# Kernel optimization log

Hardware: AMD Instinct MI355X
Metric: run time of the kernel (lower is better)

## Reference

```python
import jax, jax.numpy as jnp
import numpy as np

B, C_IN, H, W = 8, 1024, 18, 80
FEAT = 1024
A = 32      # anchors per location
NCLS = 3    # classes
NREG = 13
K = 3       # kernel size
K2 = K * K
EPS = 1e-5  # BatchNorm eps


def conv2d(x, w, b):
    y = jax.lax.conv_general_dilated(x, w, (1, 1), ((1, 1), (1, 1)),
                                     dimension_numbers=('NCHW', 'OIHW', 'NCHW'))
    return y + b[None, :, None, None]


def bn_eval(x, g, b):
    # eval-mode BatchNorm2d with running_mean=0, running_var=1
    return x * (g / jnp.sqrt(1.0 + EPS))[None, :, None, None] + b[None, :, None, None]


def anchor_flatten(x, d):
    # [B, A*d, H, W] -> permute(0,2,3,1) -> [B, H*W*A, d]
    Bx, Cx, Hx, Wx = x.shape
    return jnp.transpose(x, (0, 2, 3, 1)).reshape(Bx, Hx * Wx * (Cx // d), d)


def bilinear_gather(x, py, px):
    # x: [B,C,H,W]; py/px: [B,K2,H,W] float coords -> [B,C,K2,H,W], zero outside
    Bx, Cx, Hx, Wx = x.shape
    y0 = jnp.floor(py); x0 = jnp.floor(px)
    wy1 = py - y0; wx1 = px - x0
    wy0 = 1.0 - wy1; wx0 = 1.0 - wx1
    xf = x.reshape(Bx, Cx, Hx * Wx)

    def g(yy, xx):
        valid = ((yy >= 0) & (yy < Hx) & (xx >= 0) & (xx < Wx)).astype(x.dtype)
        yc = jnp.clip(yy, 0, Hx - 1).astype(jnp.int32)
        xc = jnp.clip(xx, 0, Wx - 1).astype(jnp.int32)
        idx = (yc * Wx + xc).reshape(Bx, -1)
        vals = jax.vmap(lambda xi, ii: xi[:, ii])(xf, idx).reshape(Bx, Cx, K2, Hx, Wx)
        return vals * valid[:, None]

    return (g(y0, x0) * (wy0 * wx0)[:, None] + g(y0, x0 + 1) * (wy0 * wx1)[:, None]
            + g(y0 + 1, x0) * (wy1 * wx0)[:, None] + g(y0 + 1, x0 + 1) * (wy1 * wx1)[:, None])


def mdcn(x, off_w, off_b, w, b):
    # ModulatedDeformConvPack (DCNv2): 3x3 conv -> (dy, dx, mask), then modulated deform conv
    out = conv2d(x, off_w, off_b)                        # [B, 3*K2, H, W]
    dy, dx, m = out[:, :K2], out[:, K2:2 * K2], jax.nn.sigmoid(out[:, 2 * K2:])
    ky, kx = jnp.meshgrid(jnp.arange(K, dtype=x.dtype), jnp.arange(K, dtype=x.dtype), indexing='ij')
    base_y = jnp.arange(x.shape[2], dtype=x.dtype)[None, None, :, None] - 1.0 + ky.reshape(1, K2, 1, 1)
    base_x = jnp.arange(x.shape[3], dtype=x.dtype)[None, None, None, :] - 1.0 + kx.reshape(1, K2, 1, 1)
    sampled = bilinear_gather(x, base_y + dy, base_x + dx) * m[:, None]   # [B,C,K2,H,W]
    O = w.shape[0]
    return jnp.einsum('bckhw,ock->bohw', sampled, w.reshape(O, w.shape[1], K2)) + b[None, :, None, None]


def setup_inputs() -> dict:
    key = jax.random.key(0)
    ks = jax.random.split(key, 10)
    s1 = 1.0 / np.sqrt(C_IN * K2)
    s2 = 1.0 / np.sqrt(FEAT * K2)
    rn = lambda k, sh, sc: jax.random.normal(k, sh, jnp.float32) * sc
    return {
        'features': jax.random.normal(ks[0], (B, C_IN, H, W), jnp.float32),
        'cls_w1': rn(ks[1], (FEAT, C_IN, K, K), s1), 'cls_b1': jnp.zeros((FEAT,), jnp.float32),
        'cls_w2': rn(ks[2], (FEAT, FEAT, K, K), s2), 'cls_b2': jnp.zeros((FEAT,), jnp.float32),
        'cls_w3': rn(ks[3], (A * NCLS, FEAT, K, K), s2), 'cls_b3': jnp.zeros((A * NCLS,), jnp.float32),
        'off_w': rn(ks[4], (3 * K2, C_IN, K, K), s1), 'off_b': jnp.zeros((3 * K2,), jnp.float32),
        'dcn_w': rn(ks[5], (FEAT, C_IN, K, K), s1), 'dcn_b': jnp.zeros((FEAT,), jnp.float32),
        'bn1_g': jnp.ones((FEAT,), jnp.float32), 'bn1_b': jnp.zeros((FEAT,), jnp.float32),
        'reg_w2': rn(ks[6], (FEAT, FEAT, K, K), s2), 'reg_b2': jnp.zeros((FEAT,), jnp.float32),
        'bn2_g': jnp.ones((FEAT,), jnp.float32), 'bn2_b': jnp.zeros((FEAT,), jnp.float32),
        'reg_w3': rn(ks[7], (A * NREG, FEAT, K, K), s2), 'reg_b3': jnp.zeros((A * NREG,), jnp.float32),
    }


def reference(features, cls_w1, cls_b1, cls_w2, cls_b2, cls_w3, cls_b3,
              off_w, off_b, dcn_w, dcn_b, bn1_g, bn1_b,
              reg_w2, reg_b2, bn2_g, bn2_b, reg_w3, reg_b3):
    # cls branch (Dropout2d is identity in eval)
    h = jax.nn.relu(conv2d(features, cls_w1, cls_b1))
    h = jax.nn.relu(conv2d(h, cls_w2, cls_b2))
    cls_preds = anchor_flatten(conv2d(h, cls_w3, cls_b3), NCLS)   # [B, H*W*A, NCLS]
    # reg branch: modulated deformable conv -> BN -> ReLU -> conv -> BN -> ReLU -> conv
    r = jax.nn.relu(bn_eval(mdcn(features, off_w, off_b, dcn_w, dcn_b), bn1_g, bn1_b))
    r = jax.nn.relu(bn_eval(conv2d(r, reg_w2, reg_b2), bn2_g, bn2_b))
    reg_preds = anchor_flatten(conv2d(r, reg_w3, reg_b3), NREG)   # [B, H*W*A, NREG]
    return (cls_preds, reg_preds)
```

## Files before the change

kernel.cpp:

```cpp
#include <hip/hip_runtime.h>
#include <math.h>

typedef short short8 __attribute__((ext_vector_type(8)));
typedef float f32x4 __attribute__((ext_vector_type(4)));
typedef unsigned short u16;
typedef unsigned int u32;

#define GAS(p) ((__attribute__((address_space(1))) void*)(p))
#define LAS(p) ((__attribute__((address_space(3))) void*)(p))

namespace {

constexpr int HW   = 1440;
constexpr int PBAT = 20 * 82 * 1024;

__device__ __forceinline__ u16 f2bf(float f) {
  u32 u = __float_as_uint(f);
  return (u16)((u + 0x7FFFu + ((u >> 16) & 1u)) >> 16);
}
__device__ __forceinline__ float bf2f(u16 h) {
  return __uint_as_float(((u32)h) << 16);
}

__device__ __forceinline__ int xcd_virt(int id, int N) {
  int q = N >> 3, r = N & 7;
  int xcd = id & 7, pos = id >> 3;
  return (xcd < r ? xcd * (q + 1) : r * (q + 1) + (xcd - r) * q) + pos;
}

__global__ __launch_bounds__(256)
void transpose_feat(const float* __restrict__ src, u16* __restrict__ dst) {
  __shared__ float tile[128][17];
  const int bh = blockIdx.y;
  const int b = bh / 18, h = bh % 18;
  const int wt = blockIdx.x % 5, ct = blockIdx.x / 5;
  const int w0 = wt * 16, c0 = ct * 128;
  const int tid = threadIdx.x;
#pragma unroll
  for (int it = 0; it < 8; ++it) {
    int idx = it * 256 + tid;
    int c = idx >> 4, w = idx & 15;
    tile[c][w] = src[((size_t)(b * 1024 + c0 + c) * 18 + h) * 80 + w0 + w];
  }
  __syncthreads();
  const int px = tid >> 4, cq = tid & 15;
  union { uint4 u; u16 s[8]; } pk;
#pragma unroll
  for (int j = 0; j < 8; ++j) pk.s[j] = f2bf(tile[cq * 8 + j][px]);
  *(uint4*)(dst + ((size_t)(b * 20 + h + 1) * 82 + (w0 + px + 1)) * 1024 + c0 + cq * 8) = pk.u;
}

struct RepackArgs {
  const float* src[7];
  u16* dst[7];
  int O[7];
  int start[7];
  int nseg;
};

__global__ __launch_bounds__(256)
void repack_all(RepackArgs ra) {
  int blk = blockIdx.x;
  int seg = 0;
#pragma unroll
  for (int i = 1; i < 7; ++i)
    if (i < ra.nseg && blk >= ra.start[i]) seg = i;
  const float* src = ra.src[seg];
  u16* dst = ra.dst[seg];
  const int O = ra.O[seg];
  int idx = (blk - ra.start[seg]) * 256 + threadIdx.x;
  if (idx >= O * 128) return;
  int o = idx >> 7, c8 = idx & 127;
  const float* s = src + (size_t)o * 9216 + (size_t)c8 * 72;
  float v[72];
#pragma unroll
  for (int i = 0; i < 18; ++i) {
    float4 f = *(const float4*)(s + i * 4);
    v[i * 4 + 0] = f.x; v[i * 4 + 1] = f.y; v[i * 4 + 2] = f.z; v[i * 4 + 3] = f.w;
  }
#pragma unroll
  for (int t = 0; t < 9; ++t) {
    union { uint4 u; u16 h[8]; } pk;
#pragma unroll
    for (int j = 0; j < 8; ++j) pk.h[j] = f2bf(v[j * 9 + t]);
    *(uint4*)(dst + ((size_t)t * O + o) * 1024 + c8 * 8) = pk.u;
  }
}

__device__ __forceinline__
void sample_body(int k, int lp, int pix0, int Npc,
                 const u16* __restrict__ featP, const float* __restrict__ offp,
                 u16* __restrict__ spl, int tid) {
  const int p = pix0 + lp;
  const int c8 = tid & 15;
  int b = p / HW, hw = p - b * HW;
  int h = hw / 80, w = hw - h * 80;
  float dy = offp[p * 27 + k];
  float dx = offp[p * 27 + 9 + k];
  float ml = offp[p * 27 + 18 + k];
  float m = 1.f / (1.f + expf(-ml));
  float py = (float)(h - 1 + k / 3) + dy;
  float px = (float)(w - 1 + (k % 3)) + dx;
  float y0f = floorf(py), x0f = floorf(px);
  float wy1 = py - y0f, wx1 = px - x0f;
  float wy0 = 1.f - wy1, wx0 = 1.f - wx1;
  int y0 = (int)y0f, x0 = (int)x0f;
  int ya = min(max(y0, -1), 18),  yb = min(max(y0 + 1, -1), 18);
  int xa = min(max(x0, -1), 80),  xb = min(max(x0 + 1, -1), 80);
  const u16* base = featP + (size_t)b * PBAT;
  const u16* r00 = base + ((size_t)(ya + 1) * 82 + (xa + 1)) * 1024;
  const u16* r01 = base + ((size_t)(ya + 1) * 82 + (xb + 1)) * 1024;
  const u16* r10 = base + ((size_t)(yb + 1) * 82 + (xa + 1)) * 1024;
  const u16* r11 = base + ((size_t)(yb + 1) * 82 + (xb + 1)) * 1024;
  float w00 = wy0 * wx0 * m, w01 = wy0 * wx1 * m;
  float w10 = wy1 * wx0 * m, w11 = wy1 * wx1 * m;
  u16* dst = spl + ((size_t)k * Npc + lp) * 1024;
  for (int c = c8 * 8; c < 1024; c += 128) {
    union { uint4 u; u16 h[8]; } a, bq, cq2, d, o;
    a.u   = *(const uint4*)(r00 + c);
    bq.u  = *(const uint4*)(r01 + c);
    cq2.u = *(const uint4*)(r10 + c);
    d.u   = *(const uint4*)(r11 + c);
#pragma unroll
    for (int j = 0; j < 8; ++j) {
      float v = w00 * bf2f(a.h[j]) + w01 * bf2f(bq.h[j]) +
                w10 * bf2f(cq2.h[j]) + w11 * bf2f(d.h[j]);
      o.h[j] = f2bf(v);
    }
    *(uint4*)(dst + c) = o.u;
  }
}

__global__ __launch_bounds__(256)
void sample_standalone(const u16* __restrict__ featP, const float* __restrict__ offp,
                       u16* __restrict__ spl, int pix0, int Npc) {
  sample_body(blockIdx.y, blockIdx.x * 16 + (threadIdx.x >> 4), pix0, Npc,
              featP, offp, spl, threadIdx.x);
}

struct Job {
  const u16* W; const u16* B;
  const float* bias; const float* bng; const float* bnb;
  void* out; int Co; int pix0; int Npc;
};

constexpr int LDSU16 = 16384;

template<int FLAGS>
__device__ __forceinline__ void gemm_body(const Job J, u16* lds, int px, int oy) {
  constexpr bool PLANES  = (FLAGS & 1) != 0;
  constexpr bool F32OUT  = (FLAGS & 2) != 0;
  constexpr bool HASBN   = (FLAGS & 4) != 0;
  constexpr bool HASRELU = (FLAGS & 8) != 0;

  u16* As = lds;
  u16* Bs = lds + 8192;
  const int tid = threadIdx.x;
  const int wv = tid >> 6, lane = tid & 63;
  const int o0 = oy * 128;
  const int p0 = J.pix0 + px * 128;

  const int lr = lane >> 2;
  const int qs = (lane & 3) ^ ((lane >> 3) & 3);
  int aoff[2], boff[2];
#pragma unroll
  for (int s = 0; s < 2; ++s) {
    int r = (wv * 2 + s) * 16 + lr;
    int o = min(o0 + r, J.Co - 1);
    aoff[s] = o * 1024 + qs * 8;
    int p = p0 + r;
    if (PLANES) {
      boff[s] = (p - J.pix0) * 1024 + qs * 8;
    } else {
      int b = p / HW, hw = p - b * HW;
      int h = hw / 80, w = hw - h * 80;
      boff[s] = ((b * 20 + h) * 82 + w) * 1024 + qs * 8;
    }
  }
  u16* aDst = As + (wv * 2) * 512;
  u16* bDst = Bs + (wv * 2) * 512;

  const int wm = wv >> 1, wn = wv & 1;
  const int frm = lane & 15;
  const int kq = lane >> 4;
  const int sel = (kq ^ ((lane >> 1) & 3)) * 16;

  f32x4 acc[4][4];
#pragma unroll
  for (int i = 0; i < 4; ++i)
#pragma unroll
    for (int j = 0; j < 4; ++j) acc[i][j] = (f32x4)0.f;

  for (int t = 0; t < 9; ++t) {
    const u16* Wt = J.W + (size_t)t * J.Co * 1024;
    const u16* Bt = J.B + (PLANES ? (size_t)t * (size_t)J.Npc * 1024
                                  : (size_t)(((t / 3) * 82 + (t % 3)) * 1024));
    for (int cc = 0; cc < 1024; cc += 64) {
      __syncthreads();
#pragma unroll
      for (int s2 = 0; s2 < 2; ++s2) {
#pragma unroll
        for (int s = 0; s < 2; ++s) {
          __builtin_amdgcn_global_load_lds(GAS(Wt + aoff[s] + cc + s2 * 32),
                                           LAS(aDst + s2 * 4096 + s * 512), 16, 0, 0);
          __builtin_amdgcn_global_load_lds(GAS(Bt + boff[s] + cc + s2 * 32),
                                           LAS(bDst + s2 * 4096 + s * 512), 16, 0, 0);
        }
      }
      __syncthreads();
#pragma unroll
      for (int s2 = 0; s2 < 2; ++s2) {
        const char* Ab = (const char*)As + s2 * 8192;
        const char* Bb = (const char*)Bs + s2 * 8192;
        uint4 af[4], bf4[4];
#pragma unroll
        for (int i = 0; i < 4; ++i) {
          af[i]  = *(const uint4*)(Ab + (wm * 64 + i * 16 + frm) * 64 + sel);
          bf4[i] = *(const uint4*)(Bb + (wn * 64 + i * 16 + frm) * 64 + sel);
        }
#pragma unroll
        for (int i = 0; i < 4; ++i) {
          short8 a = __builtin_bit_cast(short8, af[i]);
#pragma unroll
          for (int j = 0; j < 4; ++j) {
            short8 b = __builtin_bit_cast(short8, bf4[j]);
            acc[i][j] = __builtin_amdgcn_mfma_f32_16x16x32_bf16(a, b, acc[i][j], 0, 0, 0);
          }
        }
      }
    }
  }

  size_t obase[4];
#pragma unroll
  for (int j = 0; j < 4; ++j) {
    int pn = p0 + wn * 64 + j * 16 + frm;
    if (F32OUT) {
      obase[j] = (size_t)pn * J.Co;
    } else {
      int b = pn / HW, hw = pn - b * HW;
      int h = hw / 80, w = hw - h * 80;
      obase[j] = ((size_t)(b * 20 + h + 1) * 82 + (w + 1)) * 1024;
    }
  }
#pragma unroll
  for (int i = 0; i < 4; ++i) {
    int o = o0 + wm * 64 + i * 16 + kq * 4;
    float bi[4], sc[4], sh[4];
#pragma unroll
    for (int r = 0; r < 4; ++r) {
      int oc = min(o + r, J.Co - 1);
      bi[r] = J.bias[oc];
      if (HASBN) { sc[r] = J.bng[oc] * rsqrtf(1.f + 1e-5f); sh[r] = J.bnb[oc]; }
    }
#pragma unroll
    for (int j = 0; j < 4; ++j) {
      float v[4];
#pragma unroll
      for (int r = 0; r < 4; ++r) {
        float x = acc[i][j][r] + bi[r];
        if (HASBN) x = x * sc[r] + sh[r];
        if (HASRELU) x = fmaxf(x, 0.f);
        v[r] = x;
      }
      if (F32OUT) {
        float* op = (float*)J.out;
#pragma unroll
        for (int r = 0; r < 4; ++r)
          if (o + r < J.Co) op[obase[j] + o + r] = v[r];
      } else {
        u16* op = (u16*)J.out;
        ushort4 pk;
        pk.x = f2bf(v[0]); pk.y = f2bf(v[1]); pk.z = f2bf(v[2]); pk.w = f2bf(v[3]);
        *(ushort4*)(op + obase[j] + o) = pk;
      }
    }
  }
}

template<int F0, int F1>
__global__ __launch_bounds__(256)
void gemm_dual(Job j0, Job j1, int ysplit) {
  __shared__ __align__(16) u16 lds[LDSU16];
  int id = blockIdx.y * gridDim.x + blockIdx.x;
  int virt = xcd_virt(id, gridDim.x * gridDim.y);
  int NY = gridDim.y;
  int px = virt / NY, y = virt % NY;
  if (y < ysplit) gemm_body<F0>(j0, lds, px, y);
  else            gemm_body<F1>(j1, lds, px, y - ysplit);
}

template<int F0>
__global__ __launch_bounds__(256)
void gemm_sample(Job j, const u16* __restrict__ featP, const float* __restrict__ offp,
                 u16* __restrict__ spl, int n0, int pix0s, int nps) {
  __shared__ __align__(16) u16 lds[LDSU16];
  int gx = blockIdx.x;
  if (gx < n0) {
    int virt = xcd_virt(gx, n0);
    gemm_body<F0>(j, lds, virt >> 3, virt & 7);
  } else {
    int sidx = gx - n0;
    int per = nps >> 4;
    int k = sidx / per, bs = sidx % per;
    sample_body(k, bs * 16 + ((int)threadIdx.x >> 4), pix0s, nps,
                featP, offp, spl, (int)threadIdx.x);
  }
}

template<int F0, int F1>
__global__ __launch_bounds__(256)
void dcn_chunk(Job j0, Job j1, int n0, int nt0, int n1,
               const u16* __restrict__ featP, const float* __restrict__ offp,
               u16* __restrict__ splNext, int pix0n, int npn) {
  __shared__ __align__(16) u16 lds[LDSU16];
  int x = blockIdx.x;
  if (x < n0) {
    int virt = xcd_virt(x, n0);
    gemm_body<F0>(j0, lds, virt >> 3, virt & 7);
    return;
  }
  x -= n0;
  if (x < n1) { gemm_body<F1>(j1, lds, x % 90, x / 90); return; }
  x -= n1;
  int per = npn >> 4;
  int k = x / per, bs = x % per;
  sample_body(k, bs * 16 + ((int)threadIdx.x >> 4), pix0n, npn,
              featP, offp, splNext, (int)threadIdx.x);
}

}

extern "C" void kernel_launch(void* const* d_in, const int* in_sizes, int n_in,
                              void* d_out, int out_size, void* d_ws, size_t ws_size,
                              hipStream_t stream) {
  const float* feat   = (const float*)d_in[0];
  const float* cls_w1 = (const float*)d_in[1];
  const float* cls_b1 = (const float*)d_in[2];
  const float* cls_w2 = (const float*)d_in[3];
  const float* cls_b2 = (const float*)d_in[4];
  const float* cls_w3 = (const float*)d_in[5];
  const float* cls_b3 = (const float*)d_in[6];
  const float* off_w  = (const float*)d_in[7];
  const float* off_b  = (const float*)d_in[8];
  const float* dcn_w  = (const float*)d_in[9];
  const float* dcn_b  = (const float*)d_in[10];
  const float* bn1_g  = (const float*)d_in[11];
  const float* bn1_b  = (const float*)d_in[12];
  const float* reg_w2 = (const float*)d_in[13];
  const float* reg_b2 = (const float*)d_in[14];
  const float* bn2_g  = (const float*)d_in[15];
  const float* bn2_b  = (const float*)d_in[16];
  const float* reg_w3 = (const float*)d_in[17];
  const float* reg_b3 = (const float*)d_in[18];
  float* outp = (float*)d_out;

  const size_t ACTB = 26869760;
  char* wsb = (char*)d_ws;
  u16* featP = (u16*)(wsb);
  u16* bufA  = (u16*)(wsb + ACTB);
  u16* bufB  = (u16*)(wsb + 2 * ACTB);
  u16* wts   = (u16*)(wsb + 3 * ACTB);
  float* offp = (float*)(wsb + 3 * ACTB + 85432320);
  u16* spl   = (u16*)(wsb + 3 * ACTB + 85432320 + 1244160);
  const size_t BASE = 3 * ACTB + 85432320 + 1244160;
  const size_t SPLB = (size_t)9 * 11520 * 1024 * 2;

  u16* offT = wts;
  u16* w1T  = wts + 248832;
  u16* w2T  = wts + 9686016;
  u16* w3T  = wts + 19123200;
  u16* dcnT = wts + 20007936;
  u16* r2T  = wts + 29445120;
  u16* r3T  = wts + 38882304;

  dim3 blk(256);

  hipMemsetAsync(featP, 0, 3 * ACTB, stream);
  transpose_feat<<<dim3(40, 144), blk, 0, stream>>>(feat, featP);

  {
    RepackArgs ra;
    const float* s[7] = {off_w, cls_w1, cls_w2, cls_w3, dcn_w, reg_w2, reg_w3};
    u16* d[7] = {offT, w1T, w2T, w3T, dcnT, r2T, r3T};
    int  O[7] = {27, 1024, 1024, 96, 1024, 1024, 416};
    int acc = 0;
    for (int i = 0; i < 7; ++i) {
      ra.src[i] = s[i]; ra.dst[i] = d[i]; ra.O[i] = O[i]; ra.start[i] = acc;
      acc += (O[i] * 128 + 255) / 256;
    }
    ra.nseg = 7;
    repack_all<<<dim3(acc), blk, 0, stream>>>(ra);
  }

  Job jOff  = {offT, featP, off_b, nullptr, nullptr, offp, 27, 0, 0};
  Job jCls1 = {w1T, featP, cls_b1, nullptr, nullptr, bufA, 1024, 0, 0};
  Job jCls2 = {w2T, bufA, cls_b2, nullptr, nullptr, bufB, 1024, 0, 0};
  Job jCls3 = {w3T, bufB, cls_b3, nullptr, nullptr, outp, 96, 0, 0};
  Job jReg2 = {r2T, bufA, reg_b2, bn2_g, bn2_b, bufB, 1024, 0, 0};
  Job jReg3 = {r3T, bufB, reg_b3, nullptr, nullptr, outp + 1105920, 416, 0, 0};

  size_t avail = ws_size > BASE ? ws_size - BASE : 0;

  int tch = 0;
  {
    const int cand[5] = {30, 18, 15, 10, 9};
    for (int i = 0; i < 5; ++i)
      if ((size_t)2 * cand[i] * 2359296 <= avail) { tch = cand[i]; break; }
  }

  gemm_dual<8, 2><<<dim3(90, 9), blk, 0, stream>>>(jCls1, jOff, 8);

  if (avail >= SPLB) {
    gemm_sample<8><<<dim3(720 + 6480), blk, 0, stream>>>(jCls2, featP, offp, spl, 720, 0, 11520);
    Job jDcn = {dcnT, spl, dcn_b, bn1_g, bn1_b, bufA, 1024, 0, 11520};
    gemm_dual<1 | 4 | 8, 2><<<dim3(90, 9), blk, 0, stream>>>(jDcn, jCls3, 8);
    gemm_dual<4 | 8, 4 | 8><<<dim3(90, 8), blk, 0, stream>>>(jReg2, jReg2, 8);
    gemm_dual<2, 2><<<dim3(90, 4), blk, 0, stream>>>(jReg3, jReg3, 4);
  } else if (tch > 0) {
    const int C = 90 / tch;
    const int np = tch * 128;
    u16* splA = spl;
    u16* splB = spl + (size_t)tch * 1179648;

    gemm_sample<8><<<dim3(720 + 9 * (np / 16)), blk, 0, stream>>>(
        jCls2, featP, offp, splA, 720, 0, np);
    for (int i = 0; i < C; ++i) {
      u16* sCur  = (i & 1) ? splB : splA;
      u16* sNext = (i & 1) ? splA : splB;
      Job jDcnC = {dcnT, sCur, dcn_b, bn1_g, bn1_b, bufA, 1024, i * np, np};
      int n0 = tch * 8;
      int n1 = (i == 0) ? 90 : 0;
      bool hasS = (i + 1 < C);
      int ns = hasS ? 9 * (np / 16) : 0;
      dcn_chunk<1 | 4 | 8, 2><<<dim3(n0 + n1 + ns), blk, 0, stream>>>(
          jDcnC, jCls3, n0, tch, n1,
          featP, offp, sNext, (i + 1) * np, hasS ? np : 16);
    }
    gemm_dual<4 | 8, 4 | 8><<<dim3(90, 8), blk, 0, stream>>>(jReg2, jReg2, 8);
    gemm_dual<2, 2><<<dim3(90, 4), blk, 0, stream>>>(jReg3, jReg3, 4);
  } else {
    gemm_dual<8, 8><<<dim3(90, 8), blk, 0, stream>>>(jCls2, jCls2, 8);
    int tiles = (int)(avail / 2359296);
    if (tiles < 1) tiles = 1;
    if (tiles > 90) tiles = 90;
    for (int t0 = 0; t0 < 90; t0 += tiles) {
      int nt = (90 - t0) < tiles ? (90 - t0) : tiles;
      int pix0 = t0 * 128, npp = nt * 128;
      sample_standalone<<<dim3(nt * 8, 9), blk, 0, stream>>>(featP, offp, spl, pix0, npp);
      Job jDcn = {dcnT, spl, dcn_b, bn1_g, bn1_b, bufA, 1024, pix0, npp};
      gemm_dual<1 | 4 | 8, 1 | 4 | 8><<<dim3(nt, 8), blk, 0, stream>>>(jDcn, jDcn, 8);
    }
    gemm_dual<2, 2><<<dim3(90, 1), blk, 0, stream>>>(jCls3, jCls3, 1);
    gemm_dual<4 | 8, 4 | 8><<<dim3(90, 8), blk, 0, stream>>>(jReg2, jReg2, 8);
    gemm_dual<2, 2><<<dim3(90, 4), blk, 0, stream>>>(jReg3, jReg3, 4);
  }
}
```

Before: 1.980 ms.

## Double-buffer LDS in dual GEMM kernel to overlap global loads with MFMA

After: 2.189 ms. 1.11x slower.

```diff
diff --git a/kernel.cpp b/kernel.cpp
--- a/kernel.cpp
+++ b/kernel.cpp
@@ -144,97 +144,56 @@
   void* out; int Co; int pix0; int Npc;
 };
 
-constexpr int LDSU16 = 16384;
+constexpr int LDSU16  = 16384;
+constexpr int LDSU16B = 32768;
+
+struct GemmAddr {
+  int aoff[2], boff[2];
+  int wm, wn, frm, kq, sel, wv;
+};
+
+template<bool PLANES>
+__device__ __forceinline__ GemmAddr gemm_addr(const Job& J, int px, int oy) {
+  GemmAddr G;
+  const int tid = threadIdx.x;
+  G.wv = tid >> 6;
+  const int lane = tid & 63;
+  const int o0 = oy * 128;
+  const int p0 = J.pix0 + px * 128;
+  const int lr = lane >> 2;
+  const int qs = (lane & 3) ^ ((lane >> 3) & 3);
+#pragma unroll
+  for (int s = 0; s < 2; ++s) {
+    int r = (G.wv * 2 + s) * 16 + lr;
+    int o = min(o0 + r, J.Co - 1);
+    G.aoff[s] = o * 1024 + qs * 8;
+    int p = p0 + r;
+    if (PLANES) {
+      G.boff[s] = (p - J.pix0) * 1024 + qs * 8;
+    } else {
+      int b = p / HW, hw = p - b * HW;
+      int h = hw / 80, w = hw - h * 80;
+      G.boff[s] = ((b * 20 + h) * 82 + w) * 1024 + qs * 8;
+    }
+  }
+  G.wm = G.wv >> 1; G.wn = G.wv & 1;
+  G.frm = lane & 15; G.kq = lane >> 4;
+  G.sel = (G.kq ^ ((lane >> 1) & 3)) * 16;
+  return G;
+}
 
 template<int FLAGS>
-__device__ __forceinline__ void gemm_body(const Job J, u16* lds, int px, int oy) {
-  constexpr bool PLANES  = (FLAGS & 1) != 0;
+__device__ __forceinline__ void gemm_epilogue(const Job& J, const GemmAddr& G,
+                                              f32x4 (&acc)[4][4], int px, int oy) {
   constexpr bool F32OUT  = (FLAGS & 2) != 0;
   constexpr bool HASBN   = (FLAGS & 4) != 0;
   constexpr bool HASRELU = (FLAGS & 8) != 0;
-
-  u16* As = lds;
-  u16* Bs = lds + 8192;
-  const int tid = threadIdx.x;
-  const int wv = tid >> 6, lane = tid & 63;
   const int o0 = oy * 128;
   const int p0 = J.pix0 + px * 128;
-
-  const int lr = lane >> 2;
-  const int qs = (lane & 3) ^ ((lane >> 3) & 3);
-  int aoff[2], boff[2];
-#pragma unroll
-  for (int s = 0; s < 2; ++s) {
-    int r = (wv * 2 + s) * 16 + lr;
-    int o = min(o0 + r, J.Co - 1);
-    aoff[s] = o * 1024 + qs * 8;
-    int p = p0 + r;
-    if (PLANES) {
-      boff[s] = (p - J.pix0) * 1024 + qs * 8;
-    } else {
-      int b = p / HW, hw = p - b * HW;
-      int h = hw / 80, w = hw - h * 80;
-      boff[s] = ((b * 20 + h) * 82 + w) * 1024 + qs * 8;
-    }
-  }
-  u16* aDst = As + (wv * 2) * 512;
-  u16* bDst = Bs + (wv * 2) * 512;
-
-  const int wm = wv >> 1, wn = wv & 1;
-  const int frm = lane & 15;
-  const int kq = lane >> 4;
-  const int sel = (kq ^ ((lane >> 1) & 3)) * 16;
-
-  f32x4 acc[4][4];
-#pragma unroll
-  for (int i = 0; i < 4; ++i)
-#pragma unroll
-    for (int j = 0; j < 4; ++j) acc[i][j] = (f32x4)0.f;
-
-  for (int t = 0; t < 9; ++t) {
-    const u16* Wt = J.W + (size_t)t * J.Co * 1024;
-    const u16* Bt = J.B + (PLANES ? (size_t)t * (size_t)J.Npc * 1024
-                                  : (size_t)(((t / 3) * 82 + (t % 3)) * 1024));
-    for (int cc = 0; cc < 1024; cc += 64) {
-      __syncthreads();
-#pragma unroll
-      for (int s2 = 0; s2 < 2; ++s2) {
-#pragma unroll
-        for (int s = 0; s < 2; ++s) {
-          __builtin_amdgcn_global_load_lds(GAS(Wt + aoff[s] + cc + s2 * 32),
-                                           LAS(aDst + s2 * 4096 + s * 512), 16, 0, 0);
-          __builtin_amdgcn_global_load_lds(GAS(Bt + boff[s] + cc + s2 * 32),
-                                           LAS(bDst + s2 * 4096 + s * 512), 16, 0, 0);
-        }
-      }
-      __syncthreads();
-#pragma unroll
-      for (int s2 = 0; s2 < 2; ++s2) {
-        const char* Ab = (const char*)As + s2 * 8192;
-        const char* Bb = (const char*)Bs + s2 * 8192;
-        uint4 af[4], bf4[4];
-#pragma unroll
-        for (int i = 0; i < 4; ++i) {
-          af[i]  = *(const uint4*)(Ab + (wm * 64 + i * 16 + frm) * 64 + sel);
-          bf4[i] = *(const uint4*)(Bb + (wn * 64 + i * 16 + frm) * 64 + sel);
-        }
-#pragma unroll
-        for (int i = 0; i < 4; ++i) {
-          short8 a = __builtin_bit_cast(short8, af[i]);
-#pragma unroll
-          for (int j = 0; j < 4; ++j) {
-            short8 b = __builtin_bit_cast(short8, bf4[j]);
-            acc[i][j] = __builtin_amdgcn_mfma_f32_16x16x32_bf16(a, b, acc[i][j], 0, 0, 0);
-          }
-        }
-      }
-    }
-  }
-
   size_t obase[4];
 #pragma unroll
   for (int j = 0; j < 4; ++j) {
-    int pn = p0 + wn * 64 + j * 16 + frm;
+    int pn = p0 + G.wn * 64 + j * 16 + G.frm;
     if (F32OUT) {
       obase[j] = (size_t)pn * J.Co;
     } else {
@@ -245,7 +204,7 @@
   }
 #pragma unroll
   for (int i = 0; i < 4; ++i) {
-    int o = o0 + wm * 64 + i * 16 + kq * 4;
+    int o = o0 + G.wm * 64 + i * 16 + G.kq * 4;
     float bi[4], sc[4], sh[4];
 #pragma unroll
     for (int r = 0; r < 4; ++r) {
@@ -278,16 +237,136 @@
   }
 }
 
+template<int FLAGS>
+__device__ __forceinline__ void gemm_body(const Job J, u16* lds, int px, int oy) {
+  constexpr bool PLANES = (FLAGS & 1) != 0;
+  u16* As = lds;
+  u16* Bs = lds + 8192;
+  GemmAddr G = gemm_addr<PLANES>(J, px, oy);
+  u16* aDst = As + (G.wv * 2) * 512;
+  u16* bDst = Bs + (G.wv * 2) * 512;
+
+  f32x4 acc[4][4];
+#pragma unroll
+  for (int i = 0; i < 4; ++i)
+#pragma unroll
+    for (int j = 0; j < 4; ++j) acc[i][j] = (f32x4)0.f;
+
+  for (int t = 0; t < 9; ++t) {
+    const u16* Wt = J.W + (size_t)t * J.Co * 1024;
+    const u16* Bt = J.B + (PLANES ? (size_t)t * (size_t)J.Npc * 1024
+                                  : (size_t)(((t / 3) * 82 + (t % 3)) * 1024));
+    for (int cc = 0; cc < 1024; cc += 64) {
+      __syncthreads();
+#pragma unroll
+      for (int s2 = 0; s2 < 2; ++s2)
+#pragma unroll
+        for (int s = 0; s < 2; ++s) {
+          __builtin_amdgcn_global_load_lds(GAS(Wt + G.aoff[s] + cc + s2 * 32),
+                                           LAS(aDst + s2 * 4096 + s * 512), 16, 0, 0);
+          __builtin_amdgcn_global_load_lds(GAS(Bt + G.boff[s] + cc + s2 * 32),
+                                           LAS(bDst + s2 * 4096 + s * 512), 16, 0, 0);
+        }
+      __syncthreads();
+#pragma unroll
+      for (int s2 = 0; s2 < 2; ++s2) {
+        const char* Ab = (const char*)As + s2 * 8192;
+        const char* Bb = (const char*)Bs + s2 * 8192;
+        uint4 af[4], bf4[4];
+#pragma unroll
+        for (int i = 0; i < 4; ++i) {
+          af[i]  = *(const uint4*)(Ab + (G.wm * 64 + i * 16 + G.frm) * 64 + G.sel);
+          bf4[i] = *(const uint4*)(Bb + (G.wn * 64 + i * 16 + G.frm) * 64 + G.sel);
+        }
+#pragma unroll
+        for (int i = 0; i < 4; ++i) {
+          short8 a = __builtin_bit_cast(short8, af[i]);
+#pragma unroll
+          for (int j = 0; j < 4; ++j) {
+            short8 b = __builtin_bit_cast(short8, bf4[j]);
+            acc[i][j] = __builtin_amdgcn_mfma_f32_16x16x32_bf16(a, b, acc[i][j], 0, 0, 0);
+          }
+        }
+      }
+    }
+  }
+  gemm_epilogue<FLAGS>(J, G, acc, px, oy);
+}
+
+template<int FLAGS>
+__device__ __forceinline__ void gemm_body2(const Job J, u16* lds, int px, int oy) {
+  constexpr bool PLANES = (FLAGS & 1) != 0;
+  GemmAddr G = gemm_addr<PLANES>(J, px, oy);
+
+  f32x4 acc[4][4];
+#pragma unroll
+  for (int i = 0; i < 4; ++i)
+#pragma unroll
+    for (int j = 0; j < 4; ++j) acc[i][j] = (f32x4)0.f;
+
+#define G2_STAGE(BUF, KT)                                                       \
+  { int t_ = (KT) >> 4, cc_ = ((KT) & 15) << 6;                                 \
+    const u16* Wt_ = J.W + (size_t)t_ * (size_t)J.Co * 1024 + cc_;              \
+    const u16* Bt_ = J.B + (PLANES ? (size_t)t_ * (size_t)J.Npc * 1024          \
+                     : (size_t)(((t_ / 3) * 82 + (t_ % 3)) * 1024)) + cc_;      \
+    u16* aD_ = lds + (BUF) * 16384 + (G.wv * 2) * 512;                          \
+    u16* bD_ = lds + (BUF) * 16384 + 8192 + (G.wv * 2) * 512;                   \
+    _Pragma("unroll") for (int s2_ = 0; s2_ < 2; ++s2_)                         \
+    _Pragma("unroll") for (int s_ = 0; s_ < 2; ++s_) {                          \
+      __builtin_amdgcn_global_load_lds(GAS(Wt_ + G.aoff[s_] + s2_ * 32),        \
+                                       LAS(aD_ + s2_ * 4096 + s_ * 512), 16, 0, 0); \
+      __builtin_amdgcn_global_load_lds(GAS(Bt_ + G.boff[s_] + s2_ * 32),        \
+                                       LAS(bD_ + s2_ * 4096 + s_ * 512), 16, 0, 0); } }
+
+#define G2_MMA(BUF)                                                             \
+  { _Pragma("unroll") for (int s2 = 0; s2 < 2; ++s2) {                          \
+      const char* Ab = (const char*)lds + (BUF) * 32768 + s2 * 8192;            \
+      const char* Bb = (const char*)lds + (BUF) * 32768 + 16384 + s2 * 8192;    \
+      uint4 af[4], bf4[4];                                                      \
+      _Pragma("unroll") for (int i = 0; i < 4; ++i) {                           \
+        af[i]  = *(const uint4*)(Ab + (G.wm * 64 + i * 16 + G.frm) * 64 + G.sel); \
+        bf4[i] = *(const uint4*)(Bb + (G.wn * 64 + i * 16 + G.frm) * 64 + G.sel); } \
+      _Pragma("unroll") for (int i = 0; i < 4; ++i) {                           \
+        short8 a = __builtin_bit_cast(short8, af[i]);                           \
+        _Pragma("unroll") for (int j = 0; j < 4; ++j) {                         \
+          short8 b = __builtin_bit_cast(short8, bf4[j]);                        \
+          acc[i][j] = __builtin_amdgcn_mfma_f32_16x16x32_bf16(a, b, acc[i][j], 0, 0, 0); } } } }
+
+#define G2_SYNC                                                                 \
+  asm volatile("s_waitcnt vmcnt(0)" ::: "memory");                              \
+  __builtin_amdgcn_s_barrier();                                                 \
+  asm volatile("" ::: "memory");
+
+  G2_STAGE(0, 0)
+  G2_SYNC
+
+  for (int kt2 = 0; kt2 < 72; ++kt2) {
+    const int kt = kt2 * 2;
+    G2_STAGE(1, kt + 1)
+    G2_MMA(0)
+    G2_SYNC
+    if (kt2 < 71) { G2_STAGE(0, kt + 2) }
+    G2_MMA(1)
+    G2_SYNC
+  }
+
+#undef G2_STAGE
+#undef G2_MMA
+#undef G2_SYNC
+
+  gemm_epilogue<FLAGS>(J, G, acc, px, oy);
+}
+
 template<int F0, int F1>
 __global__ __launch_bounds__(256)
 void gemm_dual(Job j0, Job j1, int ysplit) {
-  __shared__ __align__(16) u16 lds[LDSU16];
+  __shared__ __align__(16) u16 lds[LDSU16B];
   int id = blockIdx.y * gridDim.x + blockIdx.x;
   int virt = xcd_virt(id, gridDim.x * gridDim.y);
   int NY = gridDim.y;
   int px = virt / NY, y = virt % NY;
-  if (y < ysplit) gemm_body<F0>(j0, lds, px, y);
-  else            gemm_body<F1>(j1, lds, px, y - ysplit);
+  if (y < ysplit) gemm_body2<F0>(j0, lds, px, y);
+  else            gemm_body2<F1>(j1, lds, px, y - ysplit);
 }
 
 template<int F0>
```
